# Optimization experiments

Hardware: AMD Instinct MI355X
Metric: run time of the kernel (lower is better)

The kernel has to match this reference:

```python
import jax, jax.numpy as jnp
import numpy as np

N, C, T, V = 16, 64, 512, 25
R, O, S = 8, 64, 3  # rel_channels, out_channels, num_subset


def setup_inputs() -> dict:
    key = jax.random.key(0)
    ks = jax.random.split(key, 12)
    sc = 0.05
    return {
        "x": jax.random.normal(ks[0], (N, C, T, V), jnp.float32),
        "A": jax.random.normal(ks[1], (S, V, V), jnp.float32) * 0.1,
        "alpha": jax.random.normal(ks[2], (1,), jnp.float32) * 0.1,
        "w1": jax.random.normal(ks[3], (S, R, C), jnp.float32) * sc,
        "b1": jax.random.normal(ks[4], (S, R), jnp.float32) * sc,
        "w2": jax.random.normal(ks[5], (S, R, C), jnp.float32) * sc,
        "b2": jax.random.normal(ks[6], (S, R), jnp.float32) * sc,
        "w3": jax.random.normal(ks[7], (S, O, C), jnp.float32) * sc,
        "b3": jax.random.normal(ks[8], (S, O), jnp.float32) * sc,
        "w4": jax.random.normal(ks[9], (S, O, R), jnp.float32) * sc,
        "b4": jax.random.normal(ks[10], (S, O), jnp.float32) * sc,
        "sparse": 0,
    }


def _mask(w, thr):
    # SparseConv2d: magnitude-threshold the 1x1 conv weights at runtime.
    return jnp.where(jnp.abs(w) > thr, w, jnp.zeros_like(w))


def reference(x, A, alpha, w1, b1, w2, b2, w3, b3, w4, b4, sparse):
    thr = jnp.float32(sparse)

    def conv1x1(w, b, inp):  # w [o,c], b [o], inp [n,c,t,v] -> [n,o,t,v]
        return jnp.einsum('oc,nctv->notv', _mask(w, thr), inp) + b[None, :, None, None]

    y = None
    for i in range(A.shape[0]):
        x1 = conv1x1(w1[i], b1[i], x).mean(-2)          # [n,r,v]
        x2 = conv1x1(w2[i], b2[i], x).mean(-2)          # [n,r,v]
        x3 = conv1x1(w3[i], b3[i], x)                   # [n,o,t,v]
        att = jnp.tanh(x1[..., :, None] - x2[..., None, :])  # [n,r,v,v]
        a = jnp.einsum('or,nruv->nouv', _mask(w4[i], thr), att) + b4[i][None, :, None, None]
        a = a * alpha + A[i][None, None]                # [n,o,v,v]
        z = jnp.einsum('ncuv,nctu->nctv', a, x3)        # node aggregation
        y = z if y is None else y + z
    # in_channels == out_channels -> residual is identity
    return jax.nn.relu(y + x)
```

## Files before the change

### kernel.cpp

```cpp
#include <hip/hip_runtime.h>
#include <cmath>

typedef __bf16 bf16x4v __attribute__((ext_vector_type(4)));
typedef __bf16 bf16x8 __attribute__((ext_vector_type(8)));
typedef float f32x4 __attribute__((ext_vector_type(4)));

namespace {
constexpr int kN = 16, kC = 64, kT = 512, kV = 25, kS = 3, kO = 64;
constexpr int kTV = kT * kV;
constexpr size_t WS_AFRAG = 102400;
constexpr size_t WS_W3F = WS_AFRAG + (size_t)48 * 131072;
}

__device__ __forceinline__ int swzA(int col, int cbyte) {
  return ((col << 7) + cbyte) ^ ((col & 7) << 4);
}
__device__ __forceinline__ int swzB(int c, int t, int ubyte) {
  return 65536 + (c << 10) + (((t << 6) + ubyte) ^ ((((c ^ t) & 7)) << 4));
}

__global__ __launch_bounds__(256) void k1_mean(const float* __restrict__ x,
                                               float* __restrict__ xm) {
  const int bid = blockIdx.x;
  __shared__ float part[250][4];
  const int tid = threadIdx.x;
  const float4* xg4 = (const float4*)(x + (size_t)bid * kTV);
  if (tid < 250) {
    float a0 = 0.f, a1 = 0.f, a2 = 0.f, a3 = 0.f;
    for (int j = tid; j < 3200; j += 250) {
      float4 v = xg4[j];
      a0 += v.x; a1 += v.y; a2 += v.z; a3 += v.w;
    }
    part[tid][0] = a0; part[tid][1] = a1; part[tid][2] = a2; part[tid][3] = a3;
  }
  __syncthreads();
  if (tid < 25) {
    float s = 0.f;
#pragma unroll
    for (int r = 0; r < 4; ++r) {
      int q = ((tid - r + 25) % 25) * 19 % 25;
#pragma unroll
      for (int p = 0; p < 10; ++p) s += part[q + 25 * p][r];
    }
    xm[bid * 25 + tid] = s * (1.f / 512.f);
  }
}

__global__ __launch_bounds__(256) void k2_attn(
    const float* __restrict__ xm, const float* __restrict__ Ag,
    const float* __restrict__ alpha, const float* __restrict__ w1,
    const float* __restrict__ b1, const float* __restrict__ w2,
    const float* __restrict__ b2, const float* __restrict__ w3,
    const float* __restrict__ w4, const float* __restrict__ b4,
    const int* __restrict__ sparse, unsigned char* __restrict__ ws) {
  const float thr = (float)sparse[0];
  const int b = blockIdx.x;
  const int s = b >> 6, n = (b >> 2) & 15, q = b & 3;
  __shared__ float xm_l[1600];
  __shared__ float x1_l[200], x2_l[200];
  __shared__ float att_l[8 * 625];
  __shared__ float attsum_l[200];
  __shared__ float ag_l[625];
  __shared__ float acs_l[25];
  __shared__ float w4_l[512];
  const int tid = threadIdx.x;
  for (int i = tid; i < 1600; i += 256) xm_l[i] = xm[n * 1600 + i];
  for (int i = tid; i < 512; i += 256) {
    float w = w4[s * 512 + i];
    w4_l[i] = (fabsf(w) > thr) ? w : 0.f;
  }
  for (int i = tid; i < 625; i += 256) ag_l[i] = Ag[s * 625 + i];
  __syncthreads();
  for (int i = tid; i < 400; i += 256) {
    int which = i / 200, idx = i % 200, r = idx / 25, u = idx % 25;
    const float* wrow = (which == 0 ? w1 : w2) + (s * 8 + r) * 64;
    float acc = 0.f;
    for (int cc = 0; cc < 64; ++cc) {
      float w = wrow[cc];
      w = (fabsf(w) > thr) ? w : 0.f;
      acc += w * xm_l[cc * 25 + u];
    }
    acc += (which == 0 ? b1 : b2)[s * 8 + r];
    if (which == 0) x1_l[idx] = acc;
    else x2_l[idx] = acc;
  }
  __syncthreads();
  for (int i = tid; i < 8 * 625; i += 256) {
    int r = i / 625, uv = i % 625, u = uv / 25, v = uv % 25;
    att_l[i] = tanhf(x1_l[r * 25 + u] - x2_l[r * 25 + v]);
  }
  __syncthreads();
  if (tid < 200) {
    int r = tid / 25, v = tid % 25;
    float sum = 0.f;
    for (int u = 0; u < 25; ++u) sum += att_l[r * 625 + u * 25 + v];
    attsum_l[tid] = sum;
  } else if (tid < 225) {
    int v = tid - 200;
    float sum = 0.f;
    for (int u = 0; u < 25; ++u) sum += ag_l[u * 25 + v];
    acs_l[v] = sum;
  }
  __syncthreads();
  const float al = alpha[0];
  unsigned char* afrag = ws + WS_AFRAG + (size_t)(s * 16 + n) * 131072;
  for (int slot = q * 2048 + tid; slot < (q + 1) * 2048; slot += 256) {
    int c = slot >> 7, vt = (slot >> 6) & 1, l = slot & 63;
    int v = vt * 16 + (l & 15), g = l >> 4;
    bf16x8 out;
    if (v < 25) {
      float b4v = b4[s * 64 + c];
#pragma unroll
      for (int j = 0; j < 8; ++j) {
        int u = g * 8 + j;
        float val = 0.f;
        if (u < 25) {
          float acc = 0.f;
#pragma unroll
          for (int r = 0; r < 8; ++r) acc += w4_l[c * 8 + r] * att_l[r * 625 + u * 25 + v];
          val = al * (acc + b4v) + ag_l[u * 25 + v];
        } else if (u == 25) {
          float acc = 0.f;
#pragma unroll
          for (int r = 0; r < 8; ++r) acc += w4_l[c * 8 + r] * attsum_l[r * 25 + v];
          val = al * acc + 25.f * al * b4v + acs_l[v];
        }
        out[j] = (__bf16)val;
      }
    } else {
#pragma unroll
      for (int j = 0; j < 8; ++j) out[j] = (__bf16)0.f;
    }
    *(bf16x8*)(afrag + (size_t)slot * 16) = out;
  }
  if (n == 0 && tid < 128) {
    unsigned char* w3f = ws + WS_W3F + (size_t)s * 8192;
    int slot = q * 128 + tid;
    int ot = slot >> 7, ks = (slot >> 6) & 1, l = slot & 63;
    int o = ot * 16 + (l & 15), g = l >> 4;
    bf16x8 out;
#pragma unroll
    for (int j = 0; j < 8; ++j) {
      int cp = ks * 32 + g * 8 + j;
      float w = w3[(s * 64 + o) * 64 + cp];
      out[j] = (__bf16)((fabsf(w) > thr) ? w : 0.f);
    }
    *(bf16x8*)(w3f + slot * 16) = out;
  }
}

__global__ __launch_bounds__(512) void k3_main(const float* __restrict__ x,
                                               const float* __restrict__ b3,
                                               const unsigned char* __restrict__ ws,
                                               float* __restrict__ y) {
  const int n = blockIdx.x;
  const int tb = blockIdx.y;
  extern __shared__ __align__(16) unsigned char smem[];
  const int tid = threadIdx.x;
  const int w = tid >> 6, l = tid & 63, g = l >> 4, l15 = l & 15;
  const float4* xg4 = (const float4*)(x + (size_t)n * kC * kTV);

  for (int idx = tid; idx < 3584; idx += 512) {
    int col_i = idx >> 3, gb = idx & 7;
    int t = col_i / 7, u = 25 + col_i % 7;
    f32x4 z = {0.f, 0.f, 0.f, 0.f};
    *(f32x4*)(smem + swzA(t * 32 + u, gb * 16)) = z;
  }
  for (int idx = tid; idx < 3072; idx += 512) {
    int pair = idx / 3, k = idx % 3;
    int c = pair >> 4, t = pair & 15;
    *(unsigned int*)(smem + swzB(c, t, 52 + 4 * k)) = 0u;
  }
  for (int i4 = tid; i4 < 6400; i4 += 512) {
    int c = i4 / 100, r4 = i4 % 100;
    float4 vv = xg4[c * 3200 + tb * 100 + r4];
    float vals[4] = {vv.x, vv.y, vv.z, vv.w};
    int lin = r4 * 4;
#pragma unroll
    for (int k = 0; k < 4; ++k) {
      int t = (lin + k) / 25, u = (lin + k) % 25;
      *(__bf16*)(smem + swzA(t * 32 + u, c * 2)) = (__bf16)vals[k];
    }
  }
  __syncthreads();

  const unsigned char* afrag = ws + WS_AFRAG;
  const unsigned char* w3f = ws + WS_W3F;

  f32x4 zacc[8][2];
#pragma unroll
  for (int cc = 0; cc < 8; ++cc)
#pragma unroll
    for (int vt = 0; vt < 2; ++vt) {
      f32x4 zz = {0.f, 0.f, 0.f, 0.f};
      zacc[cc][vt] = zz;
    }

  for (int s = 0; s < kS; ++s) {
    bf16x8 A1[4][2];
#pragma unroll
    for (int ot = 0; ot < 4; ++ot)
#pragma unroll
      for (int ks = 0; ks < 2; ++ks)
        A1[ot][ks] = *(const bf16x8*)(w3f + s * 8192 + ((ot * 2 + ks) * 64 + l) * 16);
    if (s) __syncthreads();

    f32x4 acc[4][4];
#pragma unroll
    for (int cti = 0; cti < 4; ++cti) {
      int col = w * 64 + cti * 16 + l15;
      bf16x8 xa0 = *(const bf16x8*)(smem + swzA(col, g * 16));
      bf16x8 xa1 = *(const bf16x8*)(smem + swzA(col, 64 + g * 16));
#pragma unroll
      for (int ot = 0; ot < 4; ++ot) {
        f32x4 d = {0.f, 0.f, 0.f, 0.f};
        d = __builtin_amdgcn_mfma_f32_16x16x32_bf16(xa0, A1[ot][0], d, 0, 0, 0);
        d = __builtin_amdgcn_mfma_f32_16x16x32_bf16(xa1, A1[ot][1], d, 0, 0, 0);
        acc[cti][ot] = d;
      }
    }
#pragma unroll
    for (int cti = 0; cti < 4; ++cti) {
      int t = 2 * w + (cti >> 1);
      int u0 = (cti & 1) * 16 + g * 4;
#pragma unroll
      for (int ot = 0; ot < 4; ++ot) {
        int c = ot * 16 + l15;
        if (!(cti & 1) || g < 2) {
          bf16x4v pk;
          pk[0] = (__bf16)acc[cti][ot][0];
          pk[1] = (__bf16)acc[cti][ot][1];
          pk[2] = (__bf16)acc[cti][ot][2];
          pk[3] = (__bf16)acc[cti][ot][3];
          *(bf16x4v*)(smem + swzB(c, t, 2 * u0)) = pk;
        } else if (g == 2) {
          *(__bf16*)(smem + swzB(c, t, 48)) = (__bf16)acc[cti][ot][0];
        }
      }
    }
    for (int slot = tid; slot < 1024; slot += 512) {
      int c = slot >> 4, t = slot & 15;
      *(__bf16*)(smem + swzB(c, t, 50)) = (__bf16)b3[s * 64 + c];
    }
    bf16x8 B2[8][2];
    const unsigned char* af = afrag + (size_t)(s * 16 + n) * 131072;
#pragma unroll
    for (int cc = 0; cc < 8; ++cc) {
      int c = w * 8 + cc;
#pragma unroll
      for (int vt = 0; vt < 2; ++vt)
        B2[cc][vt] = *(const bf16x8*)(af + ((c * 2 + vt) * 64 + l) * 16);
    }
    __syncthreads();
#pragma unroll
    for (int cc = 0; cc < 8; ++cc) {
      int c = w * 8 + cc;
      bf16x8 a2 = *(const bf16x8*)(smem + swzB(c, l15, g * 16));
      zacc[cc][0] = __builtin_amdgcn_mfma_f32_16x16x32_bf16(a2, B2[cc][0], zacc[cc][0], 0, 0, 0);
      zacc[cc][1] = __builtin_amdgcn_mfma_f32_16x16x32_bf16(a2, B2[cc][1], zacc[cc][1], 0, 0, 0);
    }
  }
#pragma unroll
  for (int vt = 0; vt < 2; ++vt) {
    int v = vt * 16 + l15;
#pragma unroll
    for (int jj = 0; jj < 4; ++jj) {
      int t = g * 4 + jj;
      bf16x8 xr = *(const bf16x8*)(smem + swzA(t * 32 + v, w * 16));
      if (v < 25) {
#pragma unroll
        for (int cc = 0; cc < 8; ++cc) {
          float o = fmaxf(zacc[cc][vt][jj] + (float)xr[cc], 0.f);
          y[((size_t)n * 64 + w * 8 + cc) * kTV + (tb * 16 + t) * 25 + v] = o;
        }
      }
    }
  }
}

extern "C" void kernel_launch(void* const* d_in, const int* in_sizes, int n_in,
                              void* d_out, int out_size, void* d_ws, size_t ws_size,
                              hipStream_t stream) {
  const float* x = (const float*)d_in[0];
  const float* Ag = (const float*)d_in[1];
  const float* alpha = (const float*)d_in[2];
  const float* w1 = (const float*)d_in[3];
  const float* b1 = (const float*)d_in[4];
  const float* w2 = (const float*)d_in[5];
  const float* b2 = (const float*)d_in[6];
  const float* w3 = (const float*)d_in[7];
  const float* b3 = (const float*)d_in[8];
  const float* w4 = (const float*)d_in[9];
  const float* b4 = (const float*)d_in[10];
  const int* sparse = (const int*)d_in[11];

  unsigned char* ws = (unsigned char*)d_ws;
  float* xm = (float*)ws;
  float* y = (float*)d_out;

  hipFuncSetAttribute((const void*)k3_main,
                      hipFuncAttributeMaxDynamicSharedMemorySize, 131072);

  k1_mean<<<kN * kC, 256, 0, stream>>>(x, xm);
  k2_attn<<<kS * kN * 4, 256, 0, stream>>>(xm, Ag, alpha, w1, b1, w2, b2, w3, w4,
                                           b4, sparse, ws);
  dim3 g3(kN, kT / 16);
  k3_main<<<g3, 512, 131072, stream>>>(x, b3, ws, y);
}
```

Measured before the change: 77.93 us.

## Halve k3 time tile to 8 steps and stage output through LDS for coalesced stores

The main kernel now processes 8 time steps per block instead of 16. This halves LDS use to 64KB and doubles the grid, so more blocks can be resident per CU (launch bounds now request this). The epilogue writes the fp32 aggregation result into LDS and then does coalesced float4 global loads of x and float4 stores of y. Before, the residual was read from the bf16 LDS copy and stored with scattered scalar writes. In exchange, the MFMA aggregation computes 16 time rows of which only 8 are valid (rows are aliased via l15&7), which wastes half the second-stage tensor work. The residual now uses full-precision x.

```diff
diff --git a/kernel.cpp b/kernel.cpp
--- a/kernel.cpp
+++ b/kernel.cpp
@@ -16,7 +16,7 @@
   return ((col << 7) + cbyte) ^ ((col & 7) << 4);
 }
 __device__ __forceinline__ int swzB(int c, int t, int ubyte) {
-  return 65536 + (c << 10) + (((t << 6) + ubyte) ^ ((((c ^ t) & 7)) << 4));
+  return 32768 + (c << 9) + (((t << 6) + ubyte) ^ ((((c ^ t) & 7)) << 4));
 }
 
 __global__ __launch_bounds__(256) void k1_mean(const float* __restrict__ x,
@@ -149,10 +149,10 @@
   }
 }
 
-__global__ __launch_bounds__(512) void k3_main(const float* __restrict__ x,
-                                               const float* __restrict__ b3,
-                                               const unsigned char* __restrict__ ws,
-                                               float* __restrict__ y) {
+__global__ __launch_bounds__(512, 4) void k3_main(const float* __restrict__ x,
+                                                  const float* __restrict__ b3,
+                                                  const unsigned char* __restrict__ ws,
+                                                  float* __restrict__ y) {
   const int n = blockIdx.x;
   const int tb = blockIdx.y;
   extern __shared__ __align__(16) unsigned char smem[];
@@ -160,20 +160,20 @@
   const int w = tid >> 6, l = tid & 63, g = l >> 4, l15 = l & 15;
   const float4* xg4 = (const float4*)(x + (size_t)n * kC * kTV);
 
-  for (int idx = tid; idx < 3584; idx += 512) {
+  for (int idx = tid; idx < 448; idx += 512) {
     int col_i = idx >> 3, gb = idx & 7;
     int t = col_i / 7, u = 25 + col_i % 7;
     f32x4 z = {0.f, 0.f, 0.f, 0.f};
     *(f32x4*)(smem + swzA(t * 32 + u, gb * 16)) = z;
   }
-  for (int idx = tid; idx < 3072; idx += 512) {
+  for (int idx = tid; idx < 1536; idx += 512) {
     int pair = idx / 3, k = idx % 3;
-    int c = pair >> 4, t = pair & 15;
+    int c = pair >> 3, t = pair & 7;
     *(unsigned int*)(smem + swzB(c, t, 52 + 4 * k)) = 0u;
   }
-  for (int i4 = tid; i4 < 6400; i4 += 512) {
-    int c = i4 / 100, r4 = i4 % 100;
-    float4 vv = xg4[c * 3200 + tb * 100 + r4];
+  for (int i4 = tid; i4 < 3200; i4 += 512) {
+    int c = i4 / 50, r4 = i4 % 50;
+    float4 vv = xg4[c * 3200 + tb * 50 + r4];
     float vals[4] = {vv.x, vv.y, vv.z, vv.w};
     int lin = r4 * 4;
 #pragma unroll
@@ -205,10 +205,10 @@
         A1[ot][ks] = *(const bf16x8*)(w3f + s * 8192 + ((ot * 2 + ks) * 64 + l) * 16);
     if (s) __syncthreads();
 
-    f32x4 acc[4][4];
-#pragma unroll
-    for (int cti = 0; cti < 4; ++cti) {
-      int col = w * 64 + cti * 16 + l15;
+    f32x4 acc[2][4];
+#pragma unroll
+    for (int cti = 0; cti < 2; ++cti) {
+      int col = w * 32 + cti * 16 + l15;
       bf16x8 xa0 = *(const bf16x8*)(smem + swzA(col, g * 16));
       bf16x8 xa1 = *(const bf16x8*)(smem + swzA(col, 64 + g * 16));
 #pragma unroll
@@ -220,26 +220,25 @@
       }
     }
 #pragma unroll
-    for (int cti = 0; cti < 4; ++cti) {
-      int t = 2 * w + (cti >> 1);
-      int u0 = (cti & 1) * 16 + g * 4;
+    for (int cti = 0; cti < 2; ++cti) {
+      int u0 = cti * 16 + g * 4;
 #pragma unroll
       for (int ot = 0; ot < 4; ++ot) {
         int c = ot * 16 + l15;
-        if (!(cti & 1) || g < 2) {
+        if (!cti || g < 2) {
           bf16x4v pk;
           pk[0] = (__bf16)acc[cti][ot][0];
           pk[1] = (__bf16)acc[cti][ot][1];
           pk[2] = (__bf16)acc[cti][ot][2];
           pk[3] = (__bf16)acc[cti][ot][3];
-          *(bf16x4v*)(smem + swzB(c, t, 2 * u0)) = pk;
+          *(bf16x4v*)(smem + swzB(c, w, 2 * u0)) = pk;
         } else if (g == 2) {
-          *(__bf16*)(smem + swzB(c, t, 48)) = (__bf16)acc[cti][ot][0];
+          *(__bf16*)(smem + swzB(c, w, 48)) = (__bf16)acc[cti][ot][0];
         }
       }
     }
-    for (int slot = tid; slot < 1024; slot += 512) {
-      int c = slot >> 4, t = slot & 15;
+    if (tid < 512) {
+      int c = tid >> 3, t = tid & 7;
       *(__bf16*)(smem + swzB(c, t, 50)) = (__bf16)b3[s * 64 + c];
     }
     bf16x8 B2[8][2];
@@ -255,26 +254,40 @@
 #pragma unroll
     for (int cc = 0; cc < 8; ++cc) {
       int c = w * 8 + cc;
-      bf16x8 a2 = *(const bf16x8*)(smem + swzB(c, l15, g * 16));
+      bf16x8 a2 = *(const bf16x8*)(smem + swzB(c, l15 & 7, g * 16));
       zacc[cc][0] = __builtin_amdgcn_mfma_f32_16x16x32_bf16(a2, B2[cc][0], zacc[cc][0], 0, 0, 0);
       zacc[cc][1] = __builtin_amdgcn_mfma_f32_16x16x32_bf16(a2, B2[cc][1], zacc[cc][1], 0, 0, 0);
     }
   }
-#pragma unroll
-  for (int vt = 0; vt < 2; ++vt) {
-    int v = vt * 16 + l15;
-#pragma unroll
-    for (int jj = 0; jj < 4; ++jj) {
-      int t = g * 4 + jj;
-      bf16x8 xr = *(const bf16x8*)(smem + swzA(t * 32 + v, w * 16));
-      if (v < 25) {
-#pragma unroll
-        for (int cc = 0; cc < 8; ++cc) {
-          float o = fmaxf(zacc[cc][vt][jj] + (float)xr[cc], 0.f);
-          y[((size_t)n * 64 + w * 8 + cc) * kTV + (tb * 16 + t) * 25 + v] = o;
+  __syncthreads();
+  float* zs = (float*)smem;
+  if (g < 2) {
+#pragma unroll
+    for (int cc = 0; cc < 8; ++cc) {
+      int c = w * 8 + cc;
+#pragma unroll
+      for (int vt = 0; vt < 2; ++vt) {
+        int v = vt * 16 + l15;
+        if (v < 25) {
+#pragma unroll
+          for (int jj = 0; jj < 4; ++jj)
+            zs[c * 200 + (g * 4 + jj) * 25 + v] = zacc[cc][vt][jj];
         }
       }
     }
+  }
+  __syncthreads();
+  float4* yg4 = (float4*)(y + (size_t)n * kC * kTV);
+  for (int i4 = tid; i4 < 3200; i4 += 512) {
+    int c = i4 / 50, r4 = i4 % 50;
+    float4 xv = xg4[c * 3200 + tb * 50 + r4];
+    f32x4 zv = *(const f32x4*)(zs + c * 200 + r4 * 4);
+    float4 o;
+    o.x = fmaxf(zv[0] + xv.x, 0.f);
+    o.y = fmaxf(zv[1] + xv.y, 0.f);
+    o.z = fmaxf(zv[2] + xv.z, 0.f);
+    o.w = fmaxf(zv[3] + xv.w, 0.f);
+    yg4[c * 3200 + tb * 50 + r4] = o;
   }
 }
 
@@ -299,11 +312,11 @@
   float* y = (float*)d_out;
 
   hipFuncSetAttribute((const void*)k3_main,
-                      hipFuncAttributeMaxDynamicSharedMemorySize, 131072);
+                      hipFuncAttributeMaxDynamicSharedMemorySize, 65536);
 
   k1_mean<<<kN * kC, 256, 0, stream>>>(x, xm);
   k2_attn<<<kS * kN * 4, 256, 0, stream>>>(xm, Ag, alpha, w1, b1, w2, b2, w3, w4,
                                            b4, sparse, ws);
-  dim3 g3(kN, kT / 16);
-  k3_main<<<g3, 512, 131072, stream>>>(x, b3, ws, y);
-}
+  dim3 g3(kN, kT / 8);
+  k3_main<<<g3, 512, 65536, stream>>>(x, b3, ws, y);
+}
```

Measured after the change: 146.9 us. +88.5%, slower.

## Convert x to bf16 in mean pass, load MFMA fragments directly, coalesce output

Applied to the files above, without the earlier changes.

The mean kernel now also writes a bf16 copy of x to workspace. The main kernel loads its MFMA A-fragments straight from that copy into registers instead of staging a swizzled fp32-to-bf16 tile in LDS, copies the w3 fragments into LDS, and writes the output through an LDS transpose as coalesced float4 stores. This shrinks LDS from 128KB to 88KB, which may allow more blocks per CU and cuts scattered global stores. In exchange it adds an extra bf16 write and read of x, per-element strided gathers for the fragments, and the residual now uses bf16-rounded x, which loses precision.

```diff
diff --git a/kernel.cpp b/kernel.cpp
--- a/kernel.cpp
+++ b/kernel.cpp
@@ -10,26 +10,30 @@
 constexpr int kTV = kT * kV;
 constexpr size_t WS_AFRAG = 102400;
 constexpr size_t WS_W3F = WS_AFRAG + (size_t)48 * 131072;
-}
-
-__device__ __forceinline__ int swzA(int col, int cbyte) {
-  return ((col << 7) + cbyte) ^ ((col & 7) << 4);
-}
-__device__ __forceinline__ int swzB(int c, int t, int ubyte) {
-  return 65536 + (c << 10) + (((t << 6) + ubyte) ^ ((((c ^ t) & 7)) << 4));
-}
-
-__global__ __launch_bounds__(256) void k1_mean(const float* __restrict__ x,
-                                               float* __restrict__ xm) {
+constexpr size_t WS_XBF = WS_W3F + 3 * 8192;
+}
+
+__device__ __forceinline__ int swzB16(int c, int t, int ubyte) {
+  return (c << 10) + (((t << 6) + ubyte) ^ ((((c ^ t) & 7)) << 4));
+}
+
+__global__ __launch_bounds__(256) void k1_cvt(const float* __restrict__ x,
+                                              __bf16* __restrict__ xbf,
+                                              float* __restrict__ xm) {
   const int bid = blockIdx.x;
   __shared__ float part[250][4];
   const int tid = threadIdx.x;
   const float4* xg4 = (const float4*)(x + (size_t)bid * kTV);
+  bf16x4v* xb4 = (bf16x4v*)(xbf + (size_t)bid * kTV);
   if (tid < 250) {
     float a0 = 0.f, a1 = 0.f, a2 = 0.f, a3 = 0.f;
     for (int j = tid; j < 3200; j += 250) {
       float4 v = xg4[j];
       a0 += v.x; a1 += v.y; a2 += v.z; a3 += v.w;
+      bf16x4v o;
+      o[0] = (__bf16)v.x; o[1] = (__bf16)v.y;
+      o[2] = (__bf16)v.z; o[3] = (__bf16)v.w;
+      xb4[j] = o;
     }
     part[tid][0] = a0; part[tid][1] = a1; part[tid][2] = a2; part[tid][3] = a3;
   }
@@ -149,7 +153,7 @@
   }
 }
 
-__global__ __launch_bounds__(512) void k3_main(const float* __restrict__ x,
+__global__ __launch_bounds__(512) void k3_main(const __bf16* __restrict__ xbf,
                                                const float* __restrict__ b3,
                                                const unsigned char* __restrict__ ws,
                                                float* __restrict__ y) {
@@ -158,34 +162,45 @@
   extern __shared__ __align__(16) unsigned char smem[];
   const int tid = threadIdx.x;
   const int w = tid >> 6, l = tid & 63, g = l >> 4, l15 = l & 15;
-  const float4* xg4 = (const float4*)(x + (size_t)n * kC * kTV);
-
-  for (int idx = tid; idx < 3584; idx += 512) {
-    int col_i = idx >> 3, gb = idx & 7;
-    int t = col_i / 7, u = 25 + col_i % 7;
-    f32x4 z = {0.f, 0.f, 0.f, 0.f};
-    *(f32x4*)(smem + swzA(t * 32 + u, gb * 16)) = z;
+
+  {
+    const f32x4* src = (const f32x4*)(ws + WS_W3F);
+    f32x4* dst = (f32x4*)(smem + 65536);
+    for (int i = tid; i < 1536; i += 512) dst[i] = src[i];
   }
   for (int idx = tid; idx < 3072; idx += 512) {
     int pair = idx / 3, k = idx % 3;
     int c = pair >> 4, t = pair & 15;
-    *(unsigned int*)(smem + swzB(c, t, 52 + 4 * k)) = 0u;
-  }
-  for (int i4 = tid; i4 < 6400; i4 += 512) {
-    int c = i4 / 100, r4 = i4 % 100;
-    float4 vv = xg4[c * 3200 + tb * 100 + r4];
-    float vals[4] = {vv.x, vv.y, vv.z, vv.w};
-    int lin = r4 * 4;
-#pragma unroll
-    for (int k = 0; k < 4; ++k) {
-      int t = (lin + k) / 25, u = (lin + k) % 25;
-      *(__bf16*)(smem + swzA(t * 32 + u, c * 2)) = (__bf16)vals[k];
+    *(unsigned int*)(smem + swzB16(c, t, 52 + 4 * k)) = 0u;
+  }
+
+  bf16x8 xa[4][2];
+#pragma unroll
+  for (int cti = 0; cti < 4; ++cti)
+#pragma unroll
+    for (int kf = 0; kf < 2; ++kf)
+#pragma unroll
+      for (int j = 0; j < 8; ++j) xa[cti][kf][j] = (__bf16)0.f;
+  {
+    const __bf16* xbp = xbf + (size_t)n * kC * kTV;
+#pragma unroll
+    for (int cti = 0; cti < 4; ++cti) {
+      int tt = tb * 16 + 2 * w + (cti >> 1);
+      int u = (cti & 1) * 16 + l15;
+      if (u < 25) {
+#pragma unroll
+        for (int kf = 0; kf < 2; ++kf)
+#pragma unroll
+          for (int j = 0; j < 8; ++j) {
+            int cp = kf * 32 + g * 8 + j;
+            xa[cti][kf][j] = xbp[(size_t)cp * kTV + tt * 25 + u];
+          }
+      }
     }
   }
   __syncthreads();
 
   const unsigned char* afrag = ws + WS_AFRAG;
-  const unsigned char* w3f = ws + WS_W3F;
 
   f32x4 zacc[8][2];
 #pragma unroll
@@ -197,84 +212,90 @@
     }
 
   for (int s = 0; s < kS; ++s) {
-    bf16x8 A1[4][2];
-#pragma unroll
-    for (int ot = 0; ot < 4; ++ot)
-#pragma unroll
-      for (int ks = 0; ks < 2; ++ks)
-        A1[ot][ks] = *(const bf16x8*)(w3f + s * 8192 + ((ot * 2 + ks) * 64 + l) * 16);
+    bf16x8 B2[8][2];
+    const unsigned char* af = afrag + (size_t)(s * 16 + n) * 131072;
+#pragma unroll
+    for (int cc = 0; cc < 8; ++cc) {
+      int c = w * 8 + cc;
+#pragma unroll
+      for (int vt = 0; vt < 2; ++vt)
+        B2[cc][vt] = *(const bf16x8*)(af + ((c * 2 + vt) * 64 + l) * 16);
+    }
     if (s) __syncthreads();
 
-    f32x4 acc[4][4];
-#pragma unroll
-    for (int cti = 0; cti < 4; ++cti) {
-      int col = w * 64 + cti * 16 + l15;
-      bf16x8 xa0 = *(const bf16x8*)(smem + swzA(col, g * 16));
-      bf16x8 xa1 = *(const bf16x8*)(smem + swzA(col, 64 + g * 16));
-#pragma unroll
-      for (int ot = 0; ot < 4; ++ot) {
+    const unsigned char* w3l = smem + 65536 + s * 8192;
+#pragma unroll
+    for (int ot = 0; ot < 4; ++ot) {
+      bf16x8 wk0 = *(const bf16x8*)(w3l + ((ot * 2 + 0) * 64 + l) * 16);
+      bf16x8 wk1 = *(const bf16x8*)(w3l + ((ot * 2 + 1) * 64 + l) * 16);
+      int c = ot * 16 + l15;
+#pragma unroll
+      for (int cti = 0; cti < 4; ++cti) {
         f32x4 d = {0.f, 0.f, 0.f, 0.f};
-        d = __builtin_amdgcn_mfma_f32_16x16x32_bf16(xa0, A1[ot][0], d, 0, 0, 0);
-        d = __builtin_amdgcn_mfma_f32_16x16x32_bf16(xa1, A1[ot][1], d, 0, 0, 0);
-        acc[cti][ot] = d;
-      }
-    }
-#pragma unroll
-    for (int cti = 0; cti < 4; ++cti) {
-      int t = 2 * w + (cti >> 1);
-      int u0 = (cti & 1) * 16 + g * 4;
-#pragma unroll
-      for (int ot = 0; ot < 4; ++ot) {
-        int c = ot * 16 + l15;
-        if (!(cti & 1) || g < 2) {
+        d = __builtin_amdgcn_mfma_f32_16x16x32_bf16(xa[cti][0], wk0, d, 0, 0, 0);
+        d = __builtin_amdgcn_mfma_f32_16x16x32_bf16(xa[cti][1], wk1, d, 0, 0, 0);
+        int tt = 2 * w + (cti >> 1);
+        if (!(cti & 1)) {
           bf16x4v pk;
-          pk[0] = (__bf16)acc[cti][ot][0];
-          pk[1] = (__bf16)acc[cti][ot][1];
-          pk[2] = (__bf16)acc[cti][ot][2];
-          pk[3] = (__bf16)acc[cti][ot][3];
-          *(bf16x4v*)(smem + swzB(c, t, 2 * u0)) = pk;
+          pk[0] = (__bf16)d[0]; pk[1] = (__bf16)d[1];
+          pk[2] = (__bf16)d[2]; pk[3] = (__bf16)d[3];
+          *(bf16x4v*)(smem + swzB16(c, tt, g * 8)) = pk;
+        } else if (g < 2) {
+          bf16x4v pk;
+          pk[0] = (__bf16)d[0]; pk[1] = (__bf16)d[1];
+          pk[2] = (__bf16)d[2]; pk[3] = (__bf16)d[3];
+          *(bf16x4v*)(smem + swzB16(c, tt, 32 + g * 8)) = pk;
         } else if (g == 2) {
-          *(__bf16*)(smem + swzB(c, t, 48)) = (__bf16)acc[cti][ot][0];
+          *(__bf16*)(smem + swzB16(c, tt, 48)) = (__bf16)d[0];
         }
       }
     }
-    for (int slot = tid; slot < 1024; slot += 512) {
-      int c = slot >> 4, t = slot & 15;
-      *(__bf16*)(smem + swzB(c, t, 50)) = (__bf16)b3[s * 64 + c];
-    }
-    bf16x8 B2[8][2];
-    const unsigned char* af = afrag + (size_t)(s * 16 + n) * 131072;
+    for (int i = tid; i < 1024; i += 512) {
+      int c = i >> 4, t = i & 15;
+      *(__bf16*)(smem + swzB16(c, t, 50)) = (__bf16)b3[s * 64 + c];
+    }
+    __syncthreads();
 #pragma unroll
     for (int cc = 0; cc < 8; ++cc) {
       int c = w * 8 + cc;
-#pragma unroll
-      for (int vt = 0; vt < 2; ++vt)
-        B2[cc][vt] = *(const bf16x8*)(af + ((c * 2 + vt) * 64 + l) * 16);
-    }
-    __syncthreads();
-#pragma unroll
-    for (int cc = 0; cc < 8; ++cc) {
-      int c = w * 8 + cc;
-      bf16x8 a2 = *(const bf16x8*)(smem + swzB(c, l15, g * 16));
+      bf16x8 a2 = *(const bf16x8*)(smem + swzB16(c, l15, g * 16));
       zacc[cc][0] = __builtin_amdgcn_mfma_f32_16x16x32_bf16(a2, B2[cc][0], zacc[cc][0], 0, 0, 0);
       zacc[cc][1] = __builtin_amdgcn_mfma_f32_16x16x32_bf16(a2, B2[cc][1], zacc[cc][1], 0, 0, 0);
     }
   }
-#pragma unroll
-  for (int vt = 0; vt < 2; ++vt) {
-    int v = vt * 16 + l15;
-#pragma unroll
-    for (int jj = 0; jj < 4; ++jj) {
-      int t = g * 4 + jj;
-      bf16x8 xr = *(const bf16x8*)(smem + swzA(t * 32 + v, w * 16));
-      if (v < 25) {
-#pragma unroll
-        for (int cc = 0; cc < 8; ++cc) {
-          float o = fmaxf(zacc[cc][vt][jj] + (float)xr[cc], 0.f);
-          y[((size_t)n * 64 + w * 8 + cc) * kTV + (tb * 16 + t) * 25 + v] = o;
+  __syncthreads();
+  float* zs = (float*)smem;
+  const __bf16* xbp = xbf + (size_t)n * kC * kTV;
+  float4* yg4 = (float4*)(y + (size_t)n * kC * kTV);
+#pragma unroll
+  for (int h = 0; h < 2; ++h) {
+    if ((w >> 2) == h) {
+      int c0l = (w & 3) * 8;
+#pragma unroll
+      for (int cc = 0; cc < 8; ++cc)
+#pragma unroll
+        for (int vt = 0; vt < 2; ++vt) {
+          int v = vt * 16 + l15;
+          if (v < 25) {
+#pragma unroll
+            for (int jj = 0; jj < 4; ++jj)
+              zs[(c0l + cc) * 400 + (g * 4 + jj) * 25 + v] = zacc[cc][vt][jj];
+          }
         }
-      }
-    }
+    }
+    __syncthreads();
+    for (int i4 = tid; i4 < 3200; i4 += 512) {
+      int cl = i4 / 100, r4 = i4 % 100, c = h * 32 + cl;
+      bf16x4v xv = *(const bf16x4v*)(xbp + (size_t)c * kTV + tb * 400 + r4 * 4);
+      f32x4 zv = *(const f32x4*)(zs + cl * 400 + r4 * 4);
+      float4 o;
+      o.x = fmaxf(zv[0] + (float)xv[0], 0.f);
+      o.y = fmaxf(zv[1] + (float)xv[1], 0.f);
+      o.z = fmaxf(zv[2] + (float)xv[2], 0.f);
+      o.w = fmaxf(zv[3] + (float)xv[3], 0.f);
+      yg4[c * 3200 + tb * 100 + r4] = o;
+    }
+    __syncthreads();
   }
 }
 
@@ -296,14 +317,15 @@
 
   unsigned char* ws = (unsigned char*)d_ws;
   float* xm = (float*)ws;
+  __bf16* xbf = (__bf16*)(ws + WS_XBF);
   float* y = (float*)d_out;
 
   hipFuncSetAttribute((const void*)k3_main,
-                      hipFuncAttributeMaxDynamicSharedMemorySize, 131072);
-
-  k1_mean<<<kN * kC, 256, 0, stream>>>(x, xm);
+                      hipFuncAttributeMaxDynamicSharedMemorySize, 90112);
+
+  k1_cvt<<<kN * kC, 256, 0, stream>>>(x, xbf, xm);
   k2_attn<<<kS * kN * 4, 256, 0, stream>>>(xm, Ag, alpha, w1, b1, w2, b2, w3, w4,
                                            b4, sparse, ws);
   dim3 g3(kN, kT / 16);
-  k3_main<<<g3, 512, 131072, stream>>>(x, b3, ws, y);
-}
+  k3_main<<<g3, 512, 90112, stream>>>(xbf, b3, ws, y);
+}
```

After: 74.68 us. -4.2%, faster.
